# Kernel tuning notes

Hardware: AMD Instinct MI355X
Metric: run time of the kernel (lower is better)

## Reference

```python
import jax, jax.numpy as jnp
import numpy as np
from jax import lax

N_ANCHORS = 250000
NUM_CLASSES = 80
IMG_H, IMG_W = 512, 512
K_PRE = 2000      # pre-NMS top-k candidates (static stand-in for boolean filtering)
MAX_DET = 300     # max detections returned (padded, with validity mask)
IOU_THRESH = 0.1  # nms() hardcodes thresh = 0.1
SCORE_THRESH = 0.05
BBOX_STD = (0.1, 0.1, 0.2, 0.2)


def setup_inputs() -> dict:
    key = jax.random.key(0)
    k1, k2, k3, k4, k5 = jax.random.split(key, 5)
    img_batch = jax.random.normal(k1, (1, 3, IMG_H, IMG_W), dtype=jnp.float32)
    # well-formed anchors: x1<x2, y1<y2, inside the image
    ctr = jax.random.uniform(k2, (1, N_ANCHORS, 2), minval=0.0, maxval=float(IMG_W))
    wh = jax.random.uniform(k3, (1, N_ANCHORS, 2), minval=16.0, maxval=128.0)
    anchors = jnp.concatenate([ctr - 0.5 * wh, ctr + 0.5 * wh], axis=-1).astype(jnp.float32)
    regression = jax.random.normal(k4, (1, N_ANCHORS, 4), dtype=jnp.float32)
    classification = jax.random.uniform(k5, (1, N_ANCHORS, NUM_CLASSES), dtype=jnp.float32)
    return {"img_batch": img_batch, "anchors": anchors,
            "regression": regression, "classification": classification}


def _decode_boxes(anchors, regression):
    # standard RetinaNet BBoxTransform (mean=0, std=[.1,.1,.2,.2])
    widths = anchors[..., 2] - anchors[..., 0]
    heights = anchors[..., 3] - anchors[..., 1]
    ctr_x = anchors[..., 0] + 0.5 * widths
    ctr_y = anchors[..., 1] + 0.5 * heights
    dx = regression[..., 0] * BBOX_STD[0]
    dy = regression[..., 1] * BBOX_STD[1]
    dw = regression[..., 2] * BBOX_STD[2]
    dh = regression[..., 3] * BBOX_STD[3]
    pred_ctr_x = ctr_x + dx * widths
    pred_ctr_y = ctr_y + dy * heights
    pred_w = jnp.exp(dw) * widths
    pred_h = jnp.exp(dh) * heights
    return jnp.stack([pred_ctr_x - 0.5 * pred_w, pred_ctr_y - 0.5 * pred_h,
                      pred_ctr_x + 0.5 * pred_w, pred_ctr_y + 0.5 * pred_h], axis=-1)


def _clip_boxes(boxes, height, width):
    x1 = jnp.clip(boxes[..., 0], 0.0, None)
    y1 = jnp.clip(boxes[..., 1], 0.0, None)
    x2 = jnp.clip(boxes[..., 2], None, float(width))
    y2 = jnp.clip(boxes[..., 3], None, float(height))
    return jnp.stack([x1, y1, x2, y2], axis=-1)


def _pairwise_iou(boxes):
    # boxes: [K,4] -> [K,K]
    area = (boxes[:, 2] - boxes[:, 0]) * (boxes[:, 3] - boxes[:, 1])
    xx1 = jnp.maximum(boxes[:, None, 0], boxes[None, :, 0])
    yy1 = jnp.maximum(boxes[:, None, 1], boxes[None, :, 1])
    xx2 = jnp.minimum(boxes[:, None, 2], boxes[None, :, 2])
    yy2 = jnp.minimum(boxes[:, None, 3], boxes[None, :, 3])
    inter = jnp.clip(xx2 - xx1, 0.0) * jnp.clip(yy2 - yy1, 0.0)
    return inter / (area[:, None] + area[None, :] - inter + 1e-9)


def _box_sampler(img_batch, anchors, regression, classification):
    H, W = img_batch.shape[2], img_batch.shape[3]
    boxes = _clip_boxes(_decode_boxes(anchors, regression), H, W)[0]  # [A,4]
    cls0 = classification[0]                                          # [A,C]
    scores = jnp.max(cls0, axis=-1)                                   # [A]

    # threshold mask -> top-K_PRE candidates (score sorted desc)
    cand = jnp.where(scores > SCORE_THRESH, scores, -jnp.inf)
    top_s, top_i = lax.top_k(cand, K_PRE)
    valid = jnp.isfinite(top_s)
    boxes_k = boxes[top_i]                                            # [K,4]

    # greedy NMS on sorted candidates, IoU > 0.1 suppressed
    iou = _pairwise_iou(boxes_k)                                      # [K,K]
    idx = jnp.arange(K_PRE)

    def body(i, keep):
        sup = (iou[i] > IOU_THRESH) & (idx > i) & keep[i]
        return keep & ~sup

    keep = lax.fori_loop(0, K_PRE, body, valid)

    det_s = jnp.where(keep, top_s, -jnp.inf)
    dv, di = lax.top_k(det_s, MAX_DET)
    valid_det = jnp.isfinite(dv)                                      # [MAX_DET]

    boxes_det = jnp.where(valid_det[:, None], boxes_k[di], 0.0)       # [MAX_DET,4]
    cls_det = cls0[top_i[di]]                                         # [MAX_DET,C]
    nms_scores = jnp.where(valid_det, jnp.max(cls_det, axis=-1), 0.0)
    classes = jnp.where(valid_det, jnp.argmax(cls_det, axis=-1), 0)
    selected_indices = jnp.where(valid_det, top_i[di], -1)
    return nms_scores, classes, boxes_det, selected_indices, valid_det


def reference(img_batch, anchors, regression, classification):
    return _box_sampler(img_batch, anchors, regression, classification)
```

## Files before the change

kernel.cpp:

```cpp
#include <hip/hip_runtime.h>
#include <stdint.h>

typedef unsigned long long u64;
typedef unsigned int u32;

#define NA 250000
#define NC 80
#define KP 2000
#define MD 300
#define CAP 4096
#define SCORE_TH 0.05f

#define WG __HIP_MEMORY_SCOPE_WORKGROUP


__device__ __forceinline__ u32 ald(const u32* p) {
    return __hip_atomic_load(p, __ATOMIC_RELAXED, __HIP_MEMORY_SCOPE_AGENT);
}
__device__ __forceinline__ void ast(u32* p, u32 v) {
    __hip_atomic_store(p, v, __ATOMIC_RELAXED, __HIP_MEMORY_SCOPE_AGENT);
}

__device__ __forceinline__ u64 readlane_u64(u64 v, int b) {
    u32 lo = (u32)__builtin_amdgcn_readlane((int)(u32)v, b);
    u32 hi = (u32)__builtin_amdgcn_readlane((int)(u32)(v >> 32), b);
    return ((u64)hi << 32) | lo;
}

__device__ __forceinline__ float4 decode_box(const float* __restrict__ anchors,
                                             const float* __restrict__ reg, u32 a) {
    float4 an = ((const float4*)anchors)[a];
    float4 rg = ((const float4*)reg)[a];
    float w = an.z - an.x, h = an.w - an.y;
    float cx = an.x + 0.5f * w, cy = an.y + 0.5f * h;
    float pcx = cx + (rg.x * 0.1f) * w;
    float pcy = cy + (rg.y * 0.1f) * h;
    float pw = expf(rg.z * 0.2f) * w;
    float ph = expf(rg.w * 0.2f) * h;
    float x1 = fmaxf(pcx - 0.5f * pw, 0.0f);
    float y1 = fmaxf(pcy - 0.5f * ph, 0.0f);
    float x2 = fminf(pcx + 0.5f * pw, 512.0f);
    float y2 = fminf(pcy + 0.5f * ph, 512.0f);
    return make_float4(x1, y1, x2, y2);
}

__global__ __launch_bounds__(256) void k_score(const float* __restrict__ cls,
                                               u32* __restrict__ sbits,
                                               u32* __restrict__ amax,
                                               u32* __restrict__ state,
                                               u32* __restrict__ hist0,
                                               u32* __restrict__ hist1) {
    __shared__ float vs[256 * 21];
    __shared__ unsigned short ci[256 * 21];
    int t = threadIdx.x;
    if (blockIdx.x == 0) {
        if (t < 16) state[t] = (t == 1) ? (u32)KP : 0u;
        for (int i = t; i < 2048; i += 256) { hist0[i] = 0; hist1[i] = 0; }
    }
    const int B0 = blockIdx.x * 256;
    const int base4 = B0 * 20;
    const float4* cv = (const float4*)cls;
#pragma unroll 5
    for (int r = 0; r < 20; ++r) {
        int gi = base4 + r * 256 + t;
        if (gi < NA * 20) {
            float4 v = cv[gi];
            int a = gi / 20;
            int j = gi - a * 20;
            float best = v.x; int c = 0;
            if (v.y > best) { best = v.y; c = 1; }
            if (v.z > best) { best = v.z; c = 2; }
            if (v.w > best) { best = v.w; c = 3; }
            int la = a - B0;
            vs[la * 21 + j] = best;
            ci[la * 21 + j] = (unsigned short)(j * 4 + c);
        }
    }
    __syncthreads();
    int a = B0 + t;
    if (a < NA) {
        float best = vs[t * 21]; int bi = ci[t * 21];
#pragma unroll
        for (int j = 1; j < 20; ++j) {
            float v = vs[t * 21 + j];
            if (v > best) { best = v; bi = ci[t * 21 + j]; }
        }
        sbits[a] = (best > SCORE_TH) ? __float_as_uint(best) : 0u;
        amax[a] = (u32)bi;
    }
}

__device__ __forceinline__ void pick_body(u32* state, const u32* hist, int p) {
    int lane = threadIdx.x;
    int hi = 2048 - lane * 32;
    int lo = hi - 32;
    u32 h32[32];
#pragma unroll
    for (int x = 0; x < 32; ++x) h32[x] = ald(&hist[lo + x]);
    u32 s = 0;
#pragma unroll
    for (int x = 0; x < 32; ++x) s += h32[x];
    u32 sc = s;
#pragma unroll
    for (int d = 1; d < 64; d <<= 1) {
        u32 tv = __shfl_up(sc, d);
        if (lane >= d) sc += tv;
    }
    u32 pre = sc - s;
    u32 kk = ald(&state[1]);
    if (pre < kk && kk <= sc) {
        u32 c = pre; int B = lo;
        for (int x = 31; x >= 0; --x) {
            u32 h = h32[x];
            if (c + h >= kk) { B = lo + x; ast(&state[1], kk - c); break; }
            c += h;
        }
        if (p == 0) ast(&state[0], (u32)B);
        else {
            u32 prefix = ald(&state[0]);
            ast(&state[2], ((prefix << 11) | (u32)B) << 10);
        }
    }
}

__global__ __launch_bounds__(256) void k_hist0(const u32* __restrict__ sbits,
                                               u32* hist0, u32* state) {
    __shared__ u32 lh[2048];
    __shared__ int is_last;
    int t = threadIdx.x;
    for (int i = t; i < 2048; i += 256) lh[i] = 0;
    __syncthreads();
    int idx = blockIdx.x * 1024 + t;
#pragma unroll
    for (int r = 0; r < 4; ++r) {
        int a = idx + r * 256;
        if (a < NA) atomicAdd(&lh[sbits[a] >> 21], 1u);
    }
    __syncthreads();
    for (int i = t; i < 2048; i += 256) { u32 h = lh[i]; if (h) atomicAdd(&hist0[i], h); }
    if (t == 0)
        is_last = (__hip_atomic_fetch_add(&state[5], 1u, __ATOMIC_ACQ_REL,
                                          __HIP_MEMORY_SCOPE_AGENT) == gridDim.x - 1);
    __syncthreads();
    if (is_last && t < 64) pick_body(state, hist0, 0);
}

__global__ __launch_bounds__(256) void k_hist1(const u32* __restrict__ sbits,
                                               u32* hist1, u32* state) {
    __shared__ u32 lh[2048];
    __shared__ int is_last;
    int t = threadIdx.x;
    u32 prefix = state[0];
    for (int i = t; i < 2048; i += 256) lh[i] = 0;
    __syncthreads();
    int idx = blockIdx.x * 1024 + t;
#pragma unroll
    for (int r = 0; r < 4; ++r) {
        int a = idx + r * 256;
        if (a < NA) {
            u32 bb = sbits[a];
            if ((bb >> 21) == prefix) atomicAdd(&lh[(bb >> 10) & 0x7FFu], 1u);
        }
    }
    __syncthreads();
    for (int i = t; i < 2048; i += 256) { u32 h = lh[i]; if (h) atomicAdd(&hist1[i], h); }
    if (t == 0)
        is_last = (__hip_atomic_fetch_add(&state[6], 1u, __ATOMIC_ACQ_REL,
                                          __HIP_MEMORY_SCOPE_AGENT) == gridDim.x - 1);
    __syncthreads();
    if (is_last && t < 64) pick_body(state, hist1, 1);
}

__global__ __launch_bounds__(256) void k_collect(const u32* __restrict__ sbits,
                                                 u32* state, u64* __restrict__ cand) {
    __shared__ u64 lbuf[1024];
    __shared__ u32 lcount;
    __shared__ u32 gbase;
    int t = threadIdx.x;
    if (t == 0) lcount = 0;
    __syncthreads();
    u32 pivot = state[2];
#pragma unroll
    for (int r = 0; r < 4; ++r) {
        int a = blockIdx.x * 256 + t + r * 65536;
        if (a < NA) {
            u32 b = sbits[a];
            if (b != 0u && b >= pivot) {
                u32 s = atomicAdd(&lcount, 1u);
                if (s < 1024u) lbuf[s] = ((u64)b << 32) | (u32)(~(u32)a);
            }
        }
    }
    __syncthreads();
    u32 n = lcount; if (n > 1024u) n = 1024u;
    if (t == 0 && n > 0) gbase = atomicAdd(&state[3], n);
    __syncthreads();
    if (n > 0) {
        u32 base = gbase;
        for (u32 i = t; i < n; i += 256) {
            u32 slot = base + i;
            if (slot < CAP) cand[slot] = lbuf[i];
        }
    }
}

__global__ __launch_bounds__(256) void k_rank(const u32* __restrict__ state,
                                              const u64* __restrict__ cand,
                                              u32* __restrict__ canda, u32* __restrict__ cands,
                                              float4* __restrict__ boxesg,
                                              const float* __restrict__ anchors,
                                              const float* __restrict__ reg) {
    __shared__ u64 tile[CAP];
    __shared__ u32 pr2[16][17];
    int t = threadIdx.x;
    int n = (int)state[3]; if (n > CAP) n = CAP;
    for (int i = t; i < CAP; i += 256) tile[i] = (i < n) ? cand[i] : 0ull;
    if (blockIdx.x == 0) {
        for (int i = n + t; i < 2048; i += 256) {
            canda[i] = 0u; cands[i] = 0u;
            boxesg[i] = make_float4(0.f, 0.f, 0.f, 0.f);
        }
    }
    __syncthreads();
    int li = t & 15, seg = t >> 4;
    u64 my = tile[blockIdx.x * 16 + li];
    u32 r = 0;
    int j0 = seg * 256;
#pragma unroll 8
    for (int j = j0; j < j0 + 256; ++j) r += (tile[j] > my) ? 1u : 0u;
    pr2[li][seg] = r;
    __syncthreads();
    if (t < 16) {
        int ci = blockIdx.x * 16 + t;
        if (ci < n) {
            u32 rk = 0;
#pragma unroll
            for (int s = 0; s < 16; ++s) rk += pr2[t][s];
            u64 kx = tile[ci];
            u32 a = ~((u32)kx);
            if (rk < 2048u) {
                canda[rk] = a;
                cands[rk] = (u32)(kx >> 32);
                boxesg[rk] = decode_box(anchors, reg, a);
            }
        }
    }
}

__global__ __launch_bounds__(256) void k_iou(const float4* __restrict__ boxesg,
                                             u64* __restrict__ supT) {
    __shared__ float4 jb[4][64];
    int t = threadIdx.x;
    int w = t >> 6, lane = t & 63;
    int W = blockIdx.x * 4 + w;
    int bi = W >> 5, bj = W & 31;
    int j0 = bj * 64;
    jb[w][lane] = boxesg[j0 + lane];
    __syncthreads();
    int i = bi * 64 + lane;
    if (i >= KP) return;
    u64 word = 0ull;
    if (bj >= bi) {
        int jn = KP - j0; if (jn > 64) jn = 64;
        float4 bx = boxesg[i];
        float ai = (bx.z - bx.x) * (bx.w - bx.y);
        for (int jj = 0; jj < jn; ++jj) {
            if (j0 + jj <= i) continue;
            float4 b2 = jb[w][jj];
            float aj = (b2.z - b2.x) * (b2.w - b2.y);
            float xx1 = fmaxf(bx.x, b2.x), yy1 = fmaxf(bx.y, b2.y);
            float xx2 = fminf(bx.z, b2.z), yy2 = fminf(bx.w, b2.w);
            float iw = xx2 - xx1; if (iw < 0.f) iw = 0.f;
            float ih = yy2 - yy1; if (ih < 0.f) ih = 0.f;
            float inter = iw * ih;
            float iou = inter / (ai + aj - inter + 1e-9f);
            if (iou > 0.1f) word |= (1ull << jj);
        }
    }
    supT[(size_t)bj * 2048 + i] = word;
}

__global__ __launch_bounds__(256, 1) void k_scan(const u64* __restrict__ supT,
                                                 const u32* __restrict__ cands,
                                                 const u32* __restrict__ canda,
                                                 const u32* __restrict__ amax,
                                                 const float4* __restrict__ boxesg,
                                                 float* __restrict__ out) {
    __shared__ u64 stage[16][4][128];
    __shared__ float scnd[2048];
    __shared__ int klist[2048];
    __shared__ int kcAt[17];
    __shared__ u32 removedLo[32], removedHi[32];
    __shared__ u32 stage_done[16];
    __shared__ u32 kdone;
    __shared__ u32 fold_done;

    int t = threadIdx.x;
    int wv = t >> 6, lane = t & 63;
    if (t < 16) stage_done[t] = 0;
    if (t < 32) { removedLo[t] = 0; removedHi[t] = 0; }
    if (t == 0) { kdone = 0; fold_done = 0; kcAt[0] = 0; }
    __syncthreads();

    if (wv >= 2) {
        for (int C = wv - 2; C < 16; C += 2) {
            u64 v[8];
#pragma unroll
            for (int w = 0; w < 4; ++w) {
                int wa = 2 * C + w;
                v[2 * w]     = supT[(size_t)wa * 2048 + 128 * C + lane];
                v[2 * w + 1] = supT[(size_t)wa * 2048 + 128 * C + 64 + lane];
            }
            float c0 = __uint_as_float(cands[128 * C + lane]);
            float c1 = __uint_as_float(cands[128 * C + 64 + lane]);
#pragma unroll
            for (int w = 0; w < 4; ++w) {
                stage[C][w][lane] = v[2 * w];
                stage[C][w][64 + lane] = v[2 * w + 1];
            }
            scnd[128 * C + lane] = c0;
            scnd[128 * C + 64 + lane] = c1;
            __hip_atomic_store(&stage_done[C], 1u, __ATOMIC_RELEASE, WG);
        }
        return;
    }

    if (wv == 1) {
        for (int C = 0; C < 15; ++C) {
            while (__hip_atomic_load(&kdone, __ATOMIC_ACQUIRE, WG) <= (u32)C) {}
            int lo = kcAt[C], hi = kcAt[C + 1];
            int n = hi - lo;
            u64 acc = 0ull;
#pragma unroll
            for (int q = 0; q < 32; ++q) {
                int row = (q < n) ? klist[lo + q] : -1;
                u64 v = (row >= 0 && lane < 32)
                      ? supT[(size_t)lane * 2048 + row] : 0ull;
                acc |= v;
            }
            for (int q = 32; q < n; ++q) {
                int row = klist[lo + q];
                if (lane < 32) acc |= supT[(size_t)lane * 2048 + row];
            }
            if (lane < 32 && acc) {
                __hip_atomic_fetch_or(&removedLo[lane], (u32)acc, __ATOMIC_RELAXED, WG);
                __hip_atomic_fetch_or(&removedHi[lane], (u32)(acc >> 32), __ATOMIC_RELAXED, WG);
            }
            __hip_atomic_store(&fold_done, (u32)(C + 1), __ATOMIC_RELEASE, WG);
        }
        return;
    }

    u64 carry0 = 0ull, carry1 = 0ull;
    int kc = 0;
    for (int C = 0; C < 16; ++C) {
        while (__hip_atomic_load(&stage_done[C], __ATOMIC_ACQUIRE, WG) == 0u) {}
        u64 m00 = stage[C][0][lane];
        u64 m01 = stage[C][1][lane];
        u64 m02 = stage[C][2][lane];
        u64 m03 = stage[C][3][lane];
        u64 m11 = stage[C][1][64 + lane];
        u64 m12 = stage[C][2][64 + lane];
        u64 m13 = stage[C][3][64 + lane];
        float cv0 = scnd[128 * C + lane];
        float cv1 = scnd[128 * C + 64 + lane];

        if (C >= 2) {
            while (__hip_atomic_load(&fold_done, __ATOMIC_ACQUIRE, WG) < (u32)(C - 1)) {}
        }
        u64 r0w = ((u64)removedHi[2 * C] << 32) | removedLo[2 * C];
        u64 r1w = ((u64)removedHi[2 * C + 1] << 32) | removedLo[2 * C + 1];
        u64 curw0 = carry0 | r0w;
        u64 curw1 = carry1 | r1w;
        u64 vm0 = __ballot(cv0 > SCORE_TH);
        u64 vm1 = __ballot(cv1 > SCORE_TH);
        if (C == 15) vm1 &= (1ull << (KP - 15 * 128 - 64)) - 1ull;

        u64 km0 = 0ull, km1 = 0ull, nc2 = 0ull, nc3 = 0ull;
        u64 rem0 = vm0 & ~curw0;
        while (rem0) {
            int bb = (int)__builtin_ctzll(rem0);
            km0 |= (1ull << bb);
            curw0 |= readlane_u64(m00, bb);
            curw1 |= readlane_u64(m01, bb);
            nc2   |= readlane_u64(m02, bb);
            nc3   |= readlane_u64(m03, bb);
            rem0 &= ~curw0;
            rem0 &= ~(1ull << bb);
        }
        u64 rem1 = vm1 & ~curw1;
        while (rem1) {
            int bb = (int)__builtin_ctzll(rem1);
            km1 |= (1ull << bb);
            curw1 |= readlane_u64(m11, bb);
            nc2   |= readlane_u64(m12, bb);
            nc3   |= readlane_u64(m13, bb);
            rem1 &= ~curw1;
            rem1 &= ~(1ull << bb);
        }

        int base = C * 128;
        int n0 = (int)__popcll(km0);
        if ((km0 >> lane) & 1ull)
            klist[kc + (int)__popcll(km0 & ((1ull << lane) - 1ull))] = base + lane;
        if ((km1 >> lane) & 1ull)
            klist[kc + n0 + (int)__popcll(km1 & ((1ull << lane) - 1ull))] = base + 64 + lane;
        kc += n0 + (int)__popcll(km1);
        if (lane == 0) kcAt[C + 1] = kc;
        carry0 = nc2; carry1 = nc3;
        __hip_atomic_store(&kdone, (u32)(C + 1), __ATOMIC_RELEASE, WG);

        if (kc >= MD) {
            if (lane == 0) {
                for (int C2 = C + 1; C2 < 16; ++C2) kcAt[C2 + 1] = kc;
            }
            __hip_atomic_store(&kdone, 16u, __ATOMIC_RELEASE, WG);
            break;
        }
    }

    int myci[5];
    u32 mya[5];
#pragma unroll
    for (int r = 0; r < 5; ++r) {
        int s = lane + r * 64;
        myci[r] = (s < MD && s < kc) ? klist[s] : -1;
    }
#pragma unroll
    for (int r = 0; r < 5; ++r) mya[r] = (myci[r] >= 0) ? canda[myci[r]] : 0u;
#pragma unroll
    for (int r = 0; r < 5; ++r) {
        int s = lane + r * 64;
        if (s >= MD) continue;
        if (myci[r] >= 0) {
            int ci = myci[r];
            u32 a = mya[r];
            u32 aa = (a >= NA) ? 0u : a;
            float4 bx = boxesg[ci];
            out[s] = __uint_as_float(cands[ci]);
            out[MD + s] = (float)amax[aa];
            out[2 * MD + 4 * s + 0] = bx.x;
            out[2 * MD + 4 * s + 1] = bx.y;
            out[2 * MD + 4 * s + 2] = bx.z;
            out[2 * MD + 4 * s + 3] = bx.w;
            out[6 * MD + s] = (float)a;
            out[7 * MD + s] = 1.0f;
        } else {
            out[s] = 0.f;
            out[MD + s] = 0.f;
            out[2 * MD + 4 * s + 0] = 0.f;
            out[2 * MD + 4 * s + 1] = 0.f;
            out[2 * MD + 4 * s + 2] = 0.f;
            out[2 * MD + 4 * s + 3] = 0.f;
            out[6 * MD + s] = -1.0f;
            out[7 * MD + s] = 0.f;
        }
    }
}

extern "C" void kernel_launch(void* const* d_in, const int* in_sizes, int n_in,
                              void* d_out, int out_size, void* d_ws, size_t ws_size,
                              hipStream_t stream) {
    const float* anchors = (const float*)d_in[1];
    const float* reg     = (const float*)d_in[2];
    const float* cls     = (const float*)d_in[3];
    float* out = (float*)d_out;
    char* ws = (char*)d_ws;

    u32* sbits    = (u32*)(ws + 0);
    u32* amax     = (u32*)(ws + 1000000);
    u32* state    = (u32*)(ws + 2000000);
    u32* hist0    = (u32*)(ws + 2000064);
    u32* hist1    = (u32*)(ws + 2008256);
    u64* cand     = (u64*)(ws + 2016448);
    u32* canda    = (u32*)(ws + 2049216);
    u32* cands    = (u32*)(ws + 2057408);
    float4* boxesg= (float4*)(ws + 2065600);
    u64* supT     = (u64*)(ws + 2098368);

    hipLaunchKernelGGL(k_score, dim3((NA + 255) / 256), dim3(256), 0, stream,
                       cls, sbits, amax, state, hist0, hist1);
    hipLaunchKernelGGL(k_hist0, dim3((NA + 1023) / 1024), dim3(256), 0, stream,
                       sbits, hist0, state);
    hipLaunchKernelGGL(k_hist1, dim3((NA + 1023) / 1024), dim3(256), 0, stream,
                       sbits, hist1, state);
    hipLaunchKernelGGL(k_collect, dim3(256), dim3(256), 0, stream,
                       sbits, state, cand);
    hipLaunchKernelGGL(k_rank, dim3(256), dim3(256), 0, stream,
                       state, cand, canda, cands, boxesg, anchors, reg);
    hipLaunchKernelGGL(k_iou, dim3(256), dim3(256), 0, stream, boxesg, supT);
    hipLaunchKernelGGL(k_scan, dim3(1), dim3(256), 0, stream,
                       supT, cands, canda, amax, boxesg, out);
}
```

Measured before the change: 100.3 us.

## Fuse histogram passes and candidate collection into one kernel with grid barriers

Merges k_hist0, k_hist1 and k_collect into one kernel of 256 blocks. The last-arriving block publishes the picked prefix or pivot through a release flag, and every block spin-waits on that flag before starting the next phase. This removes two kernel launches and the gaps between them. In exchange it depends on all 256 blocks being resident at once, and on state[9] and state[10] being cleared between calls. It also changes the collect indexing to contiguous 1024-element chunks per block.

After: 157.2 us. +56.6%, slower.

```diff
diff --git a/kernel.cpp b/kernel.cpp
--- a/kernel.cpp
+++ b/kernel.cpp
@@ -123,14 +123,18 @@
     }
 }
 
-__global__ __launch_bounds__(256) void k_hist0(const u32* __restrict__ sbits,
-                                               u32* hist0, u32* state) {
+__global__ __launch_bounds__(256) void k_mid(const u32* __restrict__ sbits,
+                                             u32* state, u32* hist0, u32* hist1,
+                                             u64* __restrict__ cand) {
     __shared__ u32 lh[2048];
+    __shared__ u64 lbuf[1024];
+    __shared__ u32 lcount, gbase;
     __shared__ int is_last;
     int t = threadIdx.x;
+    int idx = blockIdx.x * 1024 + t;
+
     for (int i = t; i < 2048; i += 256) lh[i] = 0;
     __syncthreads();
-    int idx = blockIdx.x * 1024 + t;
 #pragma unroll
     for (int r = 0; r < 4; ++r) {
         int a = idx + r * 256;
@@ -142,18 +146,22 @@
         is_last = (__hip_atomic_fetch_add(&state[5], 1u, __ATOMIC_ACQ_REL,
                                           __HIP_MEMORY_SCOPE_AGENT) == gridDim.x - 1);
     __syncthreads();
-    if (is_last && t < 64) pick_body(state, hist0, 0);
-}
-
-__global__ __launch_bounds__(256) void k_hist1(const u32* __restrict__ sbits,
-                                               u32* hist1, u32* state) {
-    __shared__ u32 lh[2048];
-    __shared__ int is_last;
-    int t = threadIdx.x;
-    u32 prefix = state[0];
+    if (is_last) {
+        if (t < 64) pick_body(state, hist0, 0);
+        __syncthreads();
+        if (t == 0) __hip_atomic_store(&state[9], 1u, __ATOMIC_RELEASE,
+                                       __HIP_MEMORY_SCOPE_AGENT);
+    }
+    if (t == 0) {
+        while (__hip_atomic_load(&state[9], __ATOMIC_ACQUIRE,
+                                 __HIP_MEMORY_SCOPE_AGENT) == 0u)
+            __builtin_amdgcn_s_sleep(2);
+    }
+    __syncthreads();
+
+    u32 prefix = ald(&state[0]);
     for (int i = t; i < 2048; i += 256) lh[i] = 0;
     __syncthreads();
-    int idx = blockIdx.x * 1024 + t;
 #pragma unroll
     for (int r = 0; r < 4; ++r) {
         int a = idx + r * 256;
@@ -168,21 +176,25 @@
         is_last = (__hip_atomic_fetch_add(&state[6], 1u, __ATOMIC_ACQ_REL,
                                           __HIP_MEMORY_SCOPE_AGENT) == gridDim.x - 1);
     __syncthreads();
-    if (is_last && t < 64) pick_body(state, hist1, 1);
-}
-
-__global__ __launch_bounds__(256) void k_collect(const u32* __restrict__ sbits,
-                                                 u32* state, u64* __restrict__ cand) {
-    __shared__ u64 lbuf[1024];
-    __shared__ u32 lcount;
-    __shared__ u32 gbase;
-    int t = threadIdx.x;
+    if (is_last) {
+        if (t < 64) pick_body(state, hist1, 1);
+        __syncthreads();
+        if (t == 0) __hip_atomic_store(&state[10], 1u, __ATOMIC_RELEASE,
+                                       __HIP_MEMORY_SCOPE_AGENT);
+    }
+    if (t == 0) {
+        while (__hip_atomic_load(&state[10], __ATOMIC_ACQUIRE,
+                                 __HIP_MEMORY_SCOPE_AGENT) == 0u)
+            __builtin_amdgcn_s_sleep(2);
+    }
+    __syncthreads();
+
+    u32 pivot = ald(&state[2]);
     if (t == 0) lcount = 0;
     __syncthreads();
-    u32 pivot = state[2];
 #pragma unroll
     for (int r = 0; r < 4; ++r) {
-        int a = blockIdx.x * 256 + t + r * 65536;
+        int a = idx + r * 256;
         if (a < NA) {
             u32 b = sbits[a];
             if (b != 0u && b >= pivot) {
@@ -480,12 +492,8 @@
 
     hipLaunchKernelGGL(k_score, dim3((NA + 255) / 256), dim3(256), 0, stream,
                        cls, sbits, amax, state, hist0, hist1);
-    hipLaunchKernelGGL(k_hist0, dim3((NA + 1023) / 1024), dim3(256), 0, stream,
-                       sbits, hist0, state);
-    hipLaunchKernelGGL(k_hist1, dim3((NA + 1023) / 1024), dim3(256), 0, stream,
-                       sbits, hist1, state);
-    hipLaunchKernelGGL(k_collect, dim3(256), dim3(256), 0, stream,
-                       sbits, state, cand);
+    hipLaunchKernelGGL(k_mid, dim3(256), dim3(256), 0, stream,
+                       sbits, state, hist0, hist1, cand);
     hipLaunchKernelGGL(k_rank, dim3(256), dim3(256), 0, stream,
                        state, cand, canda, cands, boxesg, anchors, reg);
     hipLaunchKernelGGL(k_iou, dim3(256), dim3(256), 0, stream, boxesg, supT);
```
